# Kernel optimization log

Hardware: AMD Instinct MI355X
Metric: run time of the kernel (lower is better)

Reference implementation:

```python
import jax, jax.numpy as jnp
import numpy as np

B, C, N = 8, 128, 4096

def conv1x1(x, W, b):
    # x: [B, Cin, N], W: [Cout, Cin], b: [Cout] -> [B, Cout, N]
    return jnp.einsum('oc,bcn->bon', W, x) + b[None, :, None]

def setup_inputs() -> dict:
    key = jax.random.key(0)
    ks = jax.random.split(key, 9)
    s = 1.0 / np.sqrt(C)
    return {
        'x': jax.random.normal(ks[0], (B, C, N), dtype=jnp.float32),
        'Wq': jax.random.uniform(ks[1], (C, C), jnp.float32, -s, s),
        'bq': jax.random.uniform(ks[2], (C,), jnp.float32, -s, s),
        'Wk': jax.random.uniform(ks[3], (C, C), jnp.float32, -s, s),
        'bk': jax.random.uniform(ks[4], (C,), jnp.float32, -s, s),
        'Wv': jax.random.uniform(ks[5], (C, C), jnp.float32, -s, s),
        'bv': jax.random.uniform(ks[6], (C,), jnp.float32, -s, s),
        'Wf': jax.random.uniform(ks[7], (C, C), jnp.float32, -s, s),
        'bf': jax.random.uniform(ks[8], (C,), jnp.float32, -s, s),
    }

def reference(x, Wq, bq, Wk, bk, Wv, bv, Wf, bf):
    q = conv1x1(x, Wq, bq)  # [B, C, N]
    k = conv1x1(x, Wk, bk)
    v = conv1x1(x, Wv, bv)
    # scores[b, i, j] = sum_c q[b, c, i] * k[b, c, j]; softmax over j (no scaling, as in source)
    attn = jax.nn.softmax(jnp.einsum('bci,bcj->bij', q, k), axis=-1)  # [B, N, N]
    # out[b, c, i] = sum_j v[b, c, j] * attn[b, i, j]
    attn_out = jnp.einsum('bcj,bij->bci', v, attn)  # [B, C, N]
    return conv1x1(attn_out, Wf, bf) + x
```

## Files before the change

### kernel.cpp

```cpp
#include <hip/hip_runtime.h>
#include <cstdio>


#define BATCH 8
#define CH    128
#define NPOS  4096
#define BCN   (BATCH * CH * NPOS)
#define LOG2E 1.4426950408889634f

typedef __attribute__((ext_vector_type(8)))  short bf16x8;
typedef __attribute__((ext_vector_type(16))) float f32x16;
typedef unsigned short ushort_t;
typedef unsigned int   uint32;

#if __has_builtin(__builtin_amdgcn_exp2f)
#define EXP2(x) __builtin_amdgcn_exp2f(x)
#else
#define EXP2(x) exp2f(x)
#endif

__device__ inline ushort_t f2bf(float f) {
    uint32 u = __float_as_uint(f);
    u += 0x7FFFu + ((u >> 16) & 1u);
    return (ushort_t)(u >> 16);
}
__device__ inline float bf2f(ushort_t h) {
    return __uint_as_float(((uint32)h) << 16);
}
__device__ inline f32x16 z16() {
    f32x16 r;
#pragma unroll
    for (int i = 0; i < 16; ++i) r[i] = 0.f;
    return r;
}
__device__ inline void gl_lds16(const ushort_t* g, ushort_t* l) {
    __builtin_amdgcn_global_load_lds(
        (const __attribute__((address_space(1))) uint32*)g,
        (__attribute__((address_space(3))) uint32*)l, 16, 0, 0);
}
__device__ inline bf16x8 cvt8(const float* p, float s) {
    const float4 a = *(const float4*)p;
    const float4 c = *(const float4*)(p + 4);
    uint32 u0, u1, u2, u3;
    asm("v_cvt_pk_bf16_f32 %0, %1, %2" : "=v"(u0) : "v"(a.x * s), "v"(a.y * s));
    asm("v_cvt_pk_bf16_f32 %0, %1, %2" : "=v"(u1) : "v"(a.z * s), "v"(a.w * s));
    asm("v_cvt_pk_bf16_f32 %0, %1, %2" : "=v"(u2) : "v"(c.x * s), "v"(c.y * s));
    asm("v_cvt_pk_bf16_f32 %0, %1, %2" : "=v"(u3) : "v"(c.z * s), "v"(c.w * s));
    union { uint32 u[4]; bf16x8 v; } r;
    r.u[0] = u0; r.u[1] = u1; r.u[2] = u2; r.u[3] = u3;
    return r.v;
}
__device__ inline bf16x8 comb8(bf16x8 p0, bf16x8 p1, float s) {
    uint32 u[4];
#pragma unroll
    for (int i = 0; i < 4; ++i) {
        const float a = (bf2f((ushort_t)p0[2 * i])     + bf2f((ushort_t)p1[2 * i]))     * s;
        const float b = (bf2f((ushort_t)p0[2 * i + 1]) + bf2f((ushort_t)p1[2 * i + 1])) * s;
        asm("v_cvt_pk_bf16_f32 %0, %1, %2" : "=v"(u[i]) : "v"(a), "v"(b));
    }
    union { uint32 uu[4]; bf16x8 v; } r;
    r.uu[0] = u[0]; r.uu[1] = u[1]; r.uu[2] = u[2]; r.uu[3] = u[3];
    return r.v;
}

__global__ __launch_bounds__(256, 2)
void qkv_mfma_kernel(const float* __restrict__ x,
                     const float* __restrict__ Wq, const float* __restrict__ bq,
                     const float* __restrict__ Wk, const float* __restrict__ bk,
                     const float* __restrict__ Wv, const float* __restrict__ bv_,
                     ushort_t* __restrict__ qt, ushort_t* __restrict__ kt,
                     ushort_t* __restrict__ vb)
{
    __shared__ float    xs[32][69];
    __shared__ ushort_t xh[64][136];
    __shared__ ushort_t xl[64][136];

    const int blk = blockIdx.x;
    const int b   = blk & 7;
    const int n0  = (blk >> 3) * 64;

    const int tid = threadIdx.x;
    const int w   = tid >> 6;
    const int l   = tid & 63;
    const int l31 = l & 31;
    const int g2  = l >> 5;

    for (int c0 = 0; c0 < CH; c0 += 32) {
        __syncthreads();
        {
            const int r = tid >> 3, f4 = tid & 7;
            const size_t base = (size_t)(b * CH + c0 + r) * NPOS + n0;
            *(float4*)&xs[r][4 * f4]      = *(const float4*)&x[base + 4 * f4];
            *(float4*)&xs[r][32 + 4 * f4] = *(const float4*)&x[base + 32 + 4 * f4];
        }
        __syncthreads();
        {
            const int n = tid >> 2, oc = tid & 3;
            bf16x8 hi, lo;
#pragma unroll
            for (int m = 0; m < 8; ++m) {
                const float v = xs[oc * 8 + m][n];
                const ushort_t h = f2bf(v);
                hi[m] = (short)h;
                lo[m] = (short)f2bf(v - bf2f(h));
            }
            *(bf16x8*)&xh[n][c0 + oc * 8] = hi;
            *(bf16x8*)&xl[n][c0 + oc * 8] = lo;
        }
    }
    __syncthreads();

    f32x16 aq0 = z16(), aq1 = z16(), ak0 = z16(), ak1 = z16();
    f32x16 av0 = z16(), av1 = z16();
    const int co = w * 32 + l31;
    const size_t wrow = (size_t)co * CH;

#pragma unroll
    for (int k = 0; k < 8; ++k) {
        const int ko = k * 16 + g2 * 8;
        const bf16x8 xh0 = *(const bf16x8*)&xh[l31][ko];
        const bf16x8 xh1 = *(const bf16x8*)&xh[32 + l31][ko];
        const bf16x8 xl0 = *(const bf16x8*)&xl[l31][ko];
        const bf16x8 xl1 = *(const bf16x8*)&xl[32 + l31][ko];
        const bf16x8 wqf = cvt8(Wq + wrow + ko, 1.0f);
        const bf16x8 wkf = cvt8(Wk + wrow + ko, LOG2E);
        const bf16x8 wvf = cvt8(Wv + wrow + ko, 1.0f);

        aq0 = __builtin_amdgcn_mfma_f32_32x32x16_bf16(xh0, wqf, aq0, 0, 0, 0);
        aq0 = __builtin_amdgcn_mfma_f32_32x32x16_bf16(xl0, wqf, aq0, 0, 0, 0);
        aq1 = __builtin_amdgcn_mfma_f32_32x32x16_bf16(xh1, wqf, aq1, 0, 0, 0);
        aq1 = __builtin_amdgcn_mfma_f32_32x32x16_bf16(xl1, wqf, aq1, 0, 0, 0);
        ak0 = __builtin_amdgcn_mfma_f32_32x32x16_bf16(xh0, wkf, ak0, 0, 0, 0);
        ak0 = __builtin_amdgcn_mfma_f32_32x32x16_bf16(xl0, wkf, ak0, 0, 0, 0);
        ak1 = __builtin_amdgcn_mfma_f32_32x32x16_bf16(xh1, wkf, ak1, 0, 0, 0);
        ak1 = __builtin_amdgcn_mfma_f32_32x32x16_bf16(xl1, wkf, ak1, 0, 0, 0);
        av0 = __builtin_amdgcn_mfma_f32_32x32x16_bf16(wvf, xh0, av0, 0, 0, 0);
        av0 = __builtin_amdgcn_mfma_f32_32x32x16_bf16(wvf, xl0, av0, 0, 0, 0);
        av1 = __builtin_amdgcn_mfma_f32_32x32x16_bf16(wvf, xh1, av1, 0, 0, 0);
        av1 = __builtin_amdgcn_mfma_f32_32x32x16_bf16(wvf, xl1, av1, 0, 0, 0);
    }

    const float bqv = bq[co];
    const float bkv = bk[co] * LOG2E;
    ushort_t* qtb = qt + (size_t)b * NPOS * CH;
    ushort_t* ktb = kt + (size_t)b * NPOS * CH;
    ushort_t* vbb = vb + (size_t)b * CH * NPOS;

#pragma unroll
    for (int rg = 0; rg < 16; ++rg) {
        const int rr = (rg & 3) + 8 * (rg >> 2) + 4 * g2;
        {
            const int na = n0 + rr;
            const int nbr = n0 + 32 + rr;
            qtb[(size_t)na * CH + co]  = f2bf(aq0[rg] + bqv);
            qtb[(size_t)nbr * CH + co] = f2bf(aq1[rg] + bqv);
            ktb[(size_t)na * CH + co]  = f2bf(ak0[rg] + bkv);
            ktb[(size_t)nbr * CH + co] = f2bf(ak1[rg] + bkv);
        }
        {
            const int cov = w * 32 + rr;
            const float bvv = bv_[cov];
            vbb[(size_t)cov * NPOS + n0 + l31]      = f2bf(av0[rg] + bvv);
            vbb[(size_t)cov * NPOS + n0 + 32 + l31] = f2bf(av1[rg] + bvv);
        }
    }
}

__global__ __launch_bounds__(256, 2)
void attn_kernel(const ushort_t* __restrict__ qt, const ushort_t* __restrict__ kt,
                 const ushort_t* __restrict__ vb, ushort_t* __restrict__ pO,
                 float* __restrict__ lw)
{
    __shared__ ushort_t Sh[4 * 8192];

    const int blk = blockIdx.x;
    const int b   = blk & 7;
    const int r   = blk >> 3;
    const int it  = r & 31;
    const int sp  = r >> 5;

    const int tid = threadIdx.x;
    const int w   = tid >> 6;
    const int l   = tid & 63;
    const int l31 = l & 31;
    const int g2  = l >> 5;

    const size_t boff = (size_t)b * NPOS * CH;
    const ushort_t* qtb = qt + boff;
    const ushort_t* ktb = kt + boff;
    const ushort_t* vbb = vb + boff;

    const int i0  = it * 128;
    const int j0b = sp * (NPOS / 2);
    const int iw  = i0 + w * 32 + l31;

    auto stage = [&](int buf, int j0) {
        ushort_t* Kl = Sh + buf * 16384;
        ushort_t* Vl = Kl + 8192;
#pragma unroll
        for (int qq = 0; qq < 4; ++qq) {
            const int u = w * 256 + qq * 64 + l;
            {
                const int row = u >> 4, sl = u & 15;
                gl_lds16(ktb + (size_t)(j0 + row) * CH + ((sl ^ (row & 7)) << 3),
                         Kl + (w * 256 + qq * 64) * 8);
            }
            {
                const int c = u >> 3, sl = u & 7;
                gl_lds16(vbb + (size_t)c * NPOS + j0 + ((sl ^ (c & 7)) << 3),
                         Vl + (w * 256 + qq * 64) * 8);
            }
        }
    };

    stage(0, j0b);

    bf16x8 qa[8];
#pragma unroll
    for (int ck = 0; ck < 8; ++ck)
        qa[ck] = *(const bf16x8*)&qtb[(size_t)iw * CH + (ck * 2 + g2) * 8];

    __syncthreads();

    f32x16 o0 = z16(), o1 = z16(), o2 = z16(), o3 = z16();
    float lsum = 0.f;

    const int NT = (NPOS / 2) / 64;
    for (int t = 0; t < NT; ++t) {
        const int cur = t & 1;
        if (t + 1 < NT) stage(cur ^ 1, j0b + (t + 1) * 64);

        const ushort_t* Kl = Sh + cur * 16384;
        const ushort_t* Vl = Kl + 8192;

#pragma unroll
        for (int sub = 0; sub < 2; ++sub) {
            f32x16 sS = z16();
            const int krow  = sub * 32 + l31;
            const int kbase = krow * 128;
            const int ksw   = krow & 7;
            __builtin_amdgcn_s_setprio(1);
#pragma unroll
            for (int ck = 0; ck < 8; ++ck) {
                const bf16x8 ka =
                    *(const bf16x8*)&Kl[kbase + (((ck * 2 + g2) ^ ksw) << 3)];
                sS = __builtin_amdgcn_mfma_f32_32x32x16_bf16(ka, qa[ck], sS, 0, 0, 0);
            }
            __builtin_amdgcn_s_setprio(0);

            float p[16];
#pragma unroll
            for (int rg = 0; rg < 16; ++rg) {
                p[rg] = EXP2(sS[rg]);
                lsum += p[rg];
            }
            uint32 d[4][2];
#pragma unroll
            for (int qd = 0; qd < 4; ++qd)
#pragma unroll
                for (int td = 0; td < 2; ++td)
                    asm("v_cvt_pk_bf16_f32 %0, %1, %2"
                        : "=v"(d[qd][td])
                        : "v"(p[4 * qd + 2 * td]), "v"(p[4 * qd + 2 * td + 1]));

#pragma unroll
            for (int kcl = 0; kcl < 2; ++kcl) {
                uint32 a0 = d[2 * kcl][0], a1 = d[2 * kcl][1];
                uint32 b0 = d[2 * kcl + 1][0], b1 = d[2 * kcl + 1][1];
                asm("v_permlane32_swap_b32 %0, %1" : "+v"(a0), "+v"(b0));
                asm("v_permlane32_swap_b32 %0, %1" : "+v"(a1), "+v"(b1));
                union { uint32 u[4]; bf16x8 v; } pf;
                pf.u[0] = a0; pf.u[1] = a1; pf.u[2] = b0; pf.u[3] = b1;

                const int vsl = (sub * 2 + kcl) * 2 + g2;
                __builtin_amdgcn_s_setprio(1);
                {
                    const int c = l31;
                    const bf16x8 vv = *(const bf16x8*)&Vl[c * 64 + ((vsl ^ (c & 7)) << 3)];
                    o0 = __builtin_amdgcn_mfma_f32_32x32x16_bf16(pf.v, vv, o0, 0, 0, 0);
                }
                {
                    const int c = 32 + l31;
                    const bf16x8 vv = *(const bf16x8*)&Vl[c * 64 + ((vsl ^ (c & 7)) << 3)];
                    o1 = __builtin_amdgcn_mfma_f32_32x32x16_bf16(pf.v, vv, o1, 0, 0, 0);
                }
                {
                    const int c = 64 + l31;
                    const bf16x8 vv = *(const bf16x8*)&Vl[c * 64 + ((vsl ^ (c & 7)) << 3)];
                    o2 = __builtin_amdgcn_mfma_f32_32x32x16_bf16(pf.v, vv, o2, 0, 0, 0);
                }
                {
                    const int c = 96 + l31;
                    const bf16x8 vv = *(const bf16x8*)&Vl[c * 64 + ((vsl ^ (c & 7)) << 3)];
                    o3 = __builtin_amdgcn_mfma_f32_32x32x16_bf16(pf.v, vv, o3, 0, 0, 0);
                }
                __builtin_amdgcn_s_setprio(0);
            }
        }
        __syncthreads();
    }

    const float lpart = lsum + __shfl_xor(lsum, 32);
    ushort_t* pOb = pO + (size_t)sp * BCN + boff;
    float* lwb = lw + (size_t)sp * (BATCH * NPOS) + (size_t)b * NPOS;
#pragma unroll
    for (int rg = 0; rg < 16; ++rg) {
        const int rr = (rg & 3) + 8 * (rg >> 2) + 4 * g2;
        const int n  = i0 + w * 32 + rr;
        ushort_t* rowp = pOb + (size_t)n * CH;
        rowp[l31]      = f2bf(o0[rg]);
        rowp[32 + l31] = f2bf(o1[rg]);
        rowp[64 + l31] = f2bf(o2[rg]);
        rowp[96 + l31] = f2bf(o3[rg]);
    }
    if (l < 32) lwb[i0 + w * 32 + l] = lpart;
}

__global__ __launch_bounds__(256, 2)
void final_mfma_kernel(const ushort_t* __restrict__ pO, const float* __restrict__ lw,
                       const float* __restrict__ Wf, const float* __restrict__ bf_,
                       const float* __restrict__ x, float* __restrict__ out)
{
    const int blk = blockIdx.x;
    const int b   = blk & 7;
    const int n0  = (blk >> 3) * 64;

    const int tid = threadIdx.x;
    const int w   = tid >> 6;
    const int l   = tid & 63;
    const int l31 = l & 31;
    const int g2  = l >> 5;

    const int BN = BATCH * NPOS;
    const int co = w * 32 + l31;
    const size_t wrow = (size_t)co * CH;

    const int bn0 = b * NPOS + n0 + l31;
    const int bn1 = bn0 + 32;
    const float invl0 = 1.0f / (lw[bn0] + lw[BN + bn0]);
    const float invl1 = 1.0f / (lw[bn1] + lw[BN + bn1]);

    f32x16 a0 = z16(), a1 = z16();

#pragma unroll
    for (int k = 0; k < 8; ++k) {
        const int ko = k * 16 + g2 * 8;
        const bf16x8 wf = cvt8(Wf + wrow + ko, 1.0f);
        {
            const size_t base = (size_t)bn0 * CH + ko;
            const bf16x8 p0 = *(const bf16x8*)&pO[base];
            const bf16x8 p1 = *(const bf16x8*)&pO[base + (size_t)BCN];
            const bf16x8 aof = comb8(p0, p1, invl0);
            a0 = __builtin_amdgcn_mfma_f32_32x32x16_bf16(wf, aof, a0, 0, 0, 0);
        }
        {
            const size_t base = (size_t)bn1 * CH + ko;
            const bf16x8 p0 = *(const bf16x8*)&pO[base];
            const bf16x8 p1 = *(const bf16x8*)&pO[base + (size_t)BCN];
            const bf16x8 aof = comb8(p0, p1, invl1);
            a1 = __builtin_amdgcn_mfma_f32_32x32x16_bf16(wf, aof, a1, 0, 0, 0);
        }
    }

#pragma unroll
    for (int rg = 0; rg < 16; ++rg) {
        const int rr  = (rg & 3) + 8 * (rg >> 2) + 4 * g2;
        const int cov = w * 32 + rr;
        const float bfv = bf_[cov];
        const size_t rbase = (size_t)(b * CH + cov) * NPOS + n0;
        out[rbase + l31]      = a0[rg] + bfv + x[rbase + l31];
        out[rbase + 32 + l31] = a1[rg] + bfv + x[rbase + 32 + l31];
    }
}

extern "C" void kernel_launch(void* const* d_in, const int* in_sizes, int n_in,
                              void* d_out, int out_size, void* d_ws, size_t ws_size,
                              hipStream_t stream)
{
    (void)in_sizes; (void)n_in; (void)out_size;
    const float* x  = (const float*)d_in[0];
    const float* Wq = (const float*)d_in[1];
    const float* bq = (const float*)d_in[2];
    const float* Wk = (const float*)d_in[3];
    const float* bk = (const float*)d_in[4];
    const float* Wv = (const float*)d_in[5];
    const float* bv = (const float*)d_in[6];
    const float* Wf = (const float*)d_in[7];
    const float* bf = (const float*)d_in[8];
    float* out = (float*)d_out;

    const size_t MB = 1u << 20;
    const size_t need = 40 * MB + 256 * 1024;
    if (ws_size < need) {
        fprintf(stderr, "kernel_launch: ws_size %zu < needed %zu\n", ws_size, need);
        return;
    }
    char* wsc = (char*)d_ws;
    ushort_t* qt   = (ushort_t*)(wsc + 0);
    ushort_t* kt   = (ushort_t*)(wsc + 8 * MB);
    ushort_t* vbuf = (ushort_t*)(wsc + 16 * MB);
    ushort_t* pO   = (ushort_t*)(wsc + 24 * MB);
    float*    lw   = (float*)(wsc + 40 * MB);

    qkv_mfma_kernel<<<dim3(512), 256, 0, stream>>>(
        x, Wq, bq, Wk, bk, Wv, bv, qt, kt, vbuf);
    attn_kernel<<<dim3(512), 256, 0, stream>>>(qt, kt, vbuf, pO, lw);
    final_mfma_kernel<<<dim3(512), 256, 0, stream>>>(
        pO, lw, Wf, bf, x, out);
}
```

Baseline: 111.2 us.

## Double query rows per warp, split keys four ways, stream swizzled Q from global

Each warp in the attention kernel now handles 64 query rows instead of 32. Every K and V fragment loaded into LDS is therefore reused across two MFMA chains, which halves LDS traffic per FLOP. To keep 512 blocks, the key dimension is split into four partitions instead of two, and the final kernel sums four partial outputs and denominators. Q is written in a fragment-swizzled layout and read from global (cache) inside the inner loop rather than held in registers. This costs more partial-output memory traffic, more accumulator registers (risking spills at 2 waves), and repeated Q loads.

```diff
diff --git a/kernel.cpp b/kernel.cpp
--- a/kernel.cpp
+++ b/kernel.cpp
@@ -50,12 +50,14 @@
     r.u[0] = u0; r.u[1] = u1; r.u[2] = u2; r.u[3] = u3;
     return r.v;
 }
-__device__ inline bf16x8 comb8(bf16x8 p0, bf16x8 p1, float s) {
+__device__ inline bf16x8 comb4(bf16x8 p0, bf16x8 p1, bf16x8 p2, bf16x8 p3, float s) {
     uint32 u[4];
 #pragma unroll
     for (int i = 0; i < 4; ++i) {
-        const float a = (bf2f((ushort_t)p0[2 * i])     + bf2f((ushort_t)p1[2 * i]))     * s;
-        const float b = (bf2f((ushort_t)p0[2 * i + 1]) + bf2f((ushort_t)p1[2 * i + 1])) * s;
+        const float a = (bf2f((ushort_t)p0[2 * i]) + bf2f((ushort_t)p1[2 * i]) +
+                         bf2f((ushort_t)p2[2 * i]) + bf2f((ushort_t)p3[2 * i])) * s;
+        const float b = (bf2f((ushort_t)p0[2 * i + 1]) + bf2f((ushort_t)p1[2 * i + 1]) +
+                         bf2f((ushort_t)p2[2 * i + 1]) + bf2f((ushort_t)p3[2 * i + 1])) * s;
         asm("v_cvt_pk_bf16_f32 %0, %1, %2" : "=v"(u[i]) : "v"(a), "v"(b));
     }
     union { uint32 uu[4]; bf16x8 v; } r;
@@ -150,12 +152,16 @@
     for (int rg = 0; rg < 16; ++rg) {
         const int rr = (rg & 3) + 8 * (rg >> 2) + 4 * g2;
         {
-            const int na = n0 + rr;
-            const int nbr = n0 + 32 + rr;
-            qtb[(size_t)na * CH + co]  = f2bf(aq0[rg] + bqv);
-            qtb[(size_t)nbr * CH + co] = f2bf(aq1[rg] + bqv);
+            const int na  = n0 + rr;
+            const int nb2 = n0 + 32 + rr;
+            const uint32 offa = (uint32)(((na >> 5) * 16 + (co >> 3)) << 8) +
+                                ((na & 31) << 3) + (co & 7);
+            const uint32 offb = (uint32)(((nb2 >> 5) * 16 + (co >> 3)) << 8) +
+                                ((nb2 & 31) << 3) + (co & 7);
+            qtb[offa] = f2bf(aq0[rg] + bqv);
+            qtb[offb] = f2bf(aq1[rg] + bqv);
             ktb[(size_t)na * CH + co]  = f2bf(ak0[rg] + bkv);
-            ktb[(size_t)nbr * CH + co] = f2bf(ak1[rg] + bkv);
+            ktb[(size_t)nb2 * CH + co] = f2bf(ak1[rg] + bkv);
         }
         {
             const int cov = w * 32 + rr;
@@ -167,7 +173,7 @@
 }
 
 __global__ __launch_bounds__(256, 2)
-void attn_kernel(const ushort_t* __restrict__ qt, const ushort_t* __restrict__ kt,
+void attn_kernel(const ushort_t* __restrict__ qsw, const ushort_t* __restrict__ kt,
                  const ushort_t* __restrict__ vb, ushort_t* __restrict__ pO,
                  float* __restrict__ lw)
 {
@@ -176,8 +182,8 @@
     const int blk = blockIdx.x;
     const int b   = blk & 7;
     const int r   = blk >> 3;
-    const int it  = r & 31;
-    const int sp  = r >> 5;
+    const int it  = r & 15;
+    const int sp  = r >> 4;
 
     const int tid = threadIdx.x;
     const int w   = tid >> 6;
@@ -186,13 +192,16 @@
     const int g2  = l >> 5;
 
     const size_t boff = (size_t)b * NPOS * CH;
-    const ushort_t* qtb = qt + boff;
     const ushort_t* ktb = kt + boff;
     const ushort_t* vbb = vb + boff;
 
-    const int i0  = it * 128;
-    const int j0b = sp * (NPOS / 2);
-    const int iw  = i0 + w * 32 + l31;
+    const int i0  = it * 256;
+    const int iw0 = i0 + w * 64;
+    const int j0b = sp * (NPOS / 4);
+
+    const ushort_t* qlane = qsw + boff + (size_t)l * 8;
+    const uint32 qb0 = (uint32)(((i0 >> 5) + 2 * w) * 16) << 8;
+    const uint32 qb1 = qb0 + (16u << 8);
 
     auto stage = [&](int buf, int j0) {
         ushort_t* Kl = Sh + buf * 16384;
@@ -214,18 +223,16 @@
     };
 
     stage(0, j0b);
-
-    bf16x8 qa[8];
-#pragma unroll
-    for (int ck = 0; ck < 8; ++ck)
-        qa[ck] = *(const bf16x8*)&qtb[(size_t)iw * CH + (ck * 2 + g2) * 8];
-
     __syncthreads();
 
-    f32x16 o0 = z16(), o1 = z16(), o2 = z16(), o3 = z16();
-    float lsum = 0.f;
-
-    const int NT = (NPOS / 2) / 64;
+    f32x16 o[2][4];
+#pragma unroll
+    for (int ib = 0; ib < 2; ++ib)
+#pragma unroll
+        for (int cb = 0; cb < 4; ++cb) o[ib][cb] = z16();
+    float lsum[2] = {0.f, 0.f};
+
+    const int NT = (NPOS / 4) / 64;
     for (int t = 0; t < NT; ++t) {
         const int cur = t & 1;
         if (t + 1 < NT) stage(cur ^ 1, j0b + (t + 1) * 64);
@@ -235,64 +242,60 @@
 
 #pragma unroll
         for (int sub = 0; sub < 2; ++sub) {
-            f32x16 sS = z16();
+            f32x16 s0 = z16(), s1 = z16();
             const int krow  = sub * 32 + l31;
             const int kbase = krow * 128;
             const int ksw   = krow & 7;
-            __builtin_amdgcn_s_setprio(1);
-#pragma unroll
+#pragma unroll 2
             for (int ck = 0; ck < 8; ++ck) {
+                const bf16x8 q0 = *(const bf16x8*)&qlane[qb0 + ck * 512];
+                const bf16x8 q1 = *(const bf16x8*)&qlane[qb1 + ck * 512];
                 const bf16x8 ka =
                     *(const bf16x8*)&Kl[kbase + (((ck * 2 + g2) ^ ksw) << 3)];
-                sS = __builtin_amdgcn_mfma_f32_32x32x16_bf16(ka, qa[ck], sS, 0, 0, 0);
-            }
-            __builtin_amdgcn_s_setprio(0);
-
-            float p[16];
-#pragma unroll
-            for (int rg = 0; rg < 16; ++rg) {
-                p[rg] = EXP2(sS[rg]);
-                lsum += p[rg];
-            }
-            uint32 d[4][2];
-#pragma unroll
-            for (int qd = 0; qd < 4; ++qd)
-#pragma unroll
-                for (int td = 0; td < 2; ++td)
-                    asm("v_cvt_pk_bf16_f32 %0, %1, %2"
-                        : "=v"(d[qd][td])
-                        : "v"(p[4 * qd + 2 * td]), "v"(p[4 * qd + 2 * td + 1]));
+                s0 = __builtin_amdgcn_mfma_f32_32x32x16_bf16(ka, q0, s0, 0, 0, 0);
+                s1 = __builtin_amdgcn_mfma_f32_32x32x16_bf16(ka, q1, s1, 0, 0, 0);
+            }
+
+            uint32 d[2][4][2];
+#pragma unroll
+            for (int ib = 0; ib < 2; ++ib) {
+                float p[16];
+#pragma unroll
+                for (int rg = 0; rg < 16; ++rg) {
+                    p[rg] = EXP2(ib == 0 ? s0[rg] : s1[rg]);
+                    lsum[ib] += p[rg];
+                }
+#pragma unroll
+                for (int qd = 0; qd < 4; ++qd)
+#pragma unroll
+                    for (int td = 0; td < 2; ++td)
+                        asm("v_cvt_pk_bf16_f32 %0, %1, %2"
+                            : "=v"(d[ib][qd][td])
+                            : "v"(p[4 * qd + 2 * td]), "v"(p[4 * qd + 2 * td + 1]));
+            }
 
 #pragma unroll
             for (int kcl = 0; kcl < 2; ++kcl) {
-                uint32 a0 = d[2 * kcl][0], a1 = d[2 * kcl][1];
-                uint32 b0 = d[2 * kcl + 1][0], b1 = d[2 * kcl + 1][1];
-                asm("v_permlane32_swap_b32 %0, %1" : "+v"(a0), "+v"(b0));
-                asm("v_permlane32_swap_b32 %0, %1" : "+v"(a1), "+v"(b1));
-                union { uint32 u[4]; bf16x8 v; } pf;
-                pf.u[0] = a0; pf.u[1] = a1; pf.u[2] = b0; pf.u[3] = b1;
-
+                bf16x8 pf[2];
+#pragma unroll
+                for (int ib = 0; ib < 2; ++ib) {
+                    uint32 a0 = d[ib][2 * kcl][0],     a1 = d[ib][2 * kcl][1];
+                    uint32 b0 = d[ib][2 * kcl + 1][0], b1 = d[ib][2 * kcl + 1][1];
+                    asm("v_permlane32_swap_b32 %0, %1" : "+v"(a0), "+v"(b0));
+                    asm("v_permlane32_swap_b32 %0, %1" : "+v"(a1), "+v"(b1));
+                    union { uint32 u[4]; bf16x8 v; } pu;
+                    pu.u[0] = a0; pu.u[1] = a1; pu.u[2] = b0; pu.u[3] = b1;
+                    pf[ib] = pu.v;
+                }
                 const int vsl = (sub * 2 + kcl) * 2 + g2;
                 __builtin_amdgcn_s_setprio(1);
-                {
-                    const int c = l31;
-                    const bf16x8 vv = *(const bf16x8*)&Vl[c * 64 + ((vsl ^ (c & 7)) << 3)];
-                    o0 = __builtin_amdgcn_mfma_f32_32x32x16_bf16(pf.v, vv, o0, 0, 0, 0);
-                }
-                {
-                    const int c = 32 + l31;
-                    const bf16x8 vv = *(const bf16x8*)&Vl[c * 64 + ((vsl ^ (c & 7)) << 3)];
-                    o1 = __builtin_amdgcn_mfma_f32_32x32x16_bf16(pf.v, vv, o1, 0, 0, 0);
-                }
-                {
-                    const int c = 64 + l31;
-                    const bf16x8 vv = *(const bf16x8*)&Vl[c * 64 + ((vsl ^ (c & 7)) << 3)];
-                    o2 = __builtin_amdgcn_mfma_f32_32x32x16_bf16(pf.v, vv, o2, 0, 0, 0);
-                }
-                {
-                    const int c = 96 + l31;
-                    const bf16x8 vv = *(const bf16x8*)&Vl[c * 64 + ((vsl ^ (c & 7)) << 3)];
-                    o3 = __builtin_amdgcn_mfma_f32_32x32x16_bf16(pf.v, vv, o3, 0, 0, 0);
+#pragma unroll
+                for (int cb = 0; cb < 4; ++cb) {
+                    const int c = cb * 32 + l31;
+                    const bf16x8 vv =
+                        *(const bf16x8*)&Vl[c * 64 + ((vsl ^ (c & 7)) << 3)];
+                    o[0][cb] = __builtin_amdgcn_mfma_f32_32x32x16_bf16(pf[0], vv, o[0][cb], 0, 0, 0);
+                    o[1][cb] = __builtin_amdgcn_mfma_f32_32x32x16_bf16(pf[1], vv, o[1][cb], 0, 0, 0);
                 }
                 __builtin_amdgcn_s_setprio(0);
             }
@@ -300,20 +303,27 @@
         __syncthreads();
     }
 
-    const float lpart = lsum + __shfl_xor(lsum, 32);
+    float lp0 = lsum[0] + __shfl_xor(lsum[0], 32);
+    float lp1 = lsum[1] + __shfl_xor(lsum[1], 32);
     ushort_t* pOb = pO + (size_t)sp * BCN + boff;
     float* lwb = lw + (size_t)sp * (BATCH * NPOS) + (size_t)b * NPOS;
 #pragma unroll
     for (int rg = 0; rg < 16; ++rg) {
         const int rr = (rg & 3) + 8 * (rg >> 2) + 4 * g2;
-        const int n  = i0 + w * 32 + rr;
-        ushort_t* rowp = pOb + (size_t)n * CH;
-        rowp[l31]      = f2bf(o0[rg]);
-        rowp[32 + l31] = f2bf(o1[rg]);
-        rowp[64 + l31] = f2bf(o2[rg]);
-        rowp[96 + l31] = f2bf(o3[rg]);
-    }
-    if (l < 32) lwb[i0 + w * 32 + l] = lpart;
+#pragma unroll
+        for (int ib = 0; ib < 2; ++ib) {
+            const int n = iw0 + ib * 32 + rr;
+            ushort_t* rowp = pOb + (size_t)n * CH;
+            rowp[l31]      = f2bf(o[ib][0][rg]);
+            rowp[32 + l31] = f2bf(o[ib][1][rg]);
+            rowp[64 + l31] = f2bf(o[ib][2][rg]);
+            rowp[96 + l31] = f2bf(o[ib][3][rg]);
+        }
+    }
+    if (l < 32) {
+        lwb[iw0 + l]      = lp0;
+        lwb[iw0 + 32 + l] = lp1;
+    }
 }
 
 __global__ __launch_bounds__(256, 2)
@@ -337,8 +347,8 @@
 
     const int bn0 = b * NPOS + n0 + l31;
     const int bn1 = bn0 + 32;
-    const float invl0 = 1.0f / (lw[bn0] + lw[BN + bn0]);
-    const float invl1 = 1.0f / (lw[bn1] + lw[BN + bn1]);
+    const float invl0 = 1.0f / (lw[bn0] + lw[BN + bn0] + lw[2 * BN + bn0] + lw[3 * BN + bn0]);
+    const float invl1 = 1.0f / (lw[bn1] + lw[BN + bn1] + lw[2 * BN + bn1] + lw[3 * BN + bn1]);
 
     f32x16 a0 = z16(), a1 = z16();
 
@@ -350,14 +360,18 @@
             const size_t base = (size_t)bn0 * CH + ko;
             const bf16x8 p0 = *(const bf16x8*)&pO[base];
             const bf16x8 p1 = *(const bf16x8*)&pO[base + (size_t)BCN];
-            const bf16x8 aof = comb8(p0, p1, invl0);
+            const bf16x8 p2 = *(const bf16x8*)&pO[base + (size_t)2 * BCN];
+            const bf16x8 p3 = *(const bf16x8*)&pO[base + (size_t)3 * BCN];
+            const bf16x8 aof = comb4(p0, p1, p2, p3, invl0);
             a0 = __builtin_amdgcn_mfma_f32_32x32x16_bf16(wf, aof, a0, 0, 0, 0);
         }
         {
             const size_t base = (size_t)bn1 * CH + ko;
             const bf16x8 p0 = *(const bf16x8*)&pO[base];
             const bf16x8 p1 = *(const bf16x8*)&pO[base + (size_t)BCN];
-            const bf16x8 aof = comb8(p0, p1, invl1);
+            const bf16x8 p2 = *(const bf16x8*)&pO[base + (size_t)2 * BCN];
+            const bf16x8 p3 = *(const bf16x8*)&pO[base + (size_t)3 * BCN];
+            const bf16x8 aof = comb4(p0, p1, p2, p3, invl1);
             a1 = __builtin_amdgcn_mfma_f32_32x32x16_bf16(wf, aof, a1, 0, 0, 0);
         }
     }
@@ -390,7 +404,7 @@
     float* out = (float*)d_out;
 
     const size_t MB = 1u << 20;
-    const size_t need = 40 * MB + 256 * 1024;
+    const size_t need = 56 * MB + 512 * 1024;
     if (ws_size < need) {
         fprintf(stderr, "kernel_launch: ws_size %zu < needed %zu\n", ws_size, need);
         return;
@@ -400,7 +414,7 @@
     ushort_t* kt   = (ushort_t*)(wsc + 8 * MB);
     ushort_t* vbuf = (ushort_t*)(wsc + 16 * MB);
     ushort_t* pO   = (ushort_t*)(wsc + 24 * MB);
-    float*    lw   = (float*)(wsc + 40 * MB);
+    float*    lw   = (float*)(wsc + 56 * MB);
 
     qkv_mfma_kernel<<<dim3(512), 256, 0, stream>>>(
         x, Wq, bq, Wk, bk, Wv, bv, qt, kt, vbuf);
```

Measured after the change: 132.7 us. 1.19x slower.

## Split attention key range four ways with smaller KV tiles and higher occupancy

Applied to the files above, without the earlier changes.

The attention kernel now splits the key/value range into four partitions instead of two, doubling the grid to 1024 blocks. It also halves the per-iteration KV tile to 32 keys, shrinking LDS and raising the occupancy hint to 4 blocks per CU. The final kernel combines four partial outputs and four partial row sums. This trades more parallelism and latency hiding for twice the partial-output traffic to global memory and more sync iterations per key.

```diff
diff --git a/kernel.cpp b/kernel.cpp
--- a/kernel.cpp
+++ b/kernel.cpp
@@ -50,12 +50,14 @@
     r.u[0] = u0; r.u[1] = u1; r.u[2] = u2; r.u[3] = u3;
     return r.v;
 }
-__device__ inline bf16x8 comb8(bf16x8 p0, bf16x8 p1, float s) {
+__device__ inline bf16x8 comb4(bf16x8 p0, bf16x8 p1, bf16x8 p2, bf16x8 p3, float s) {
     uint32 u[4];
 #pragma unroll
     for (int i = 0; i < 4; ++i) {
-        const float a = (bf2f((ushort_t)p0[2 * i])     + bf2f((ushort_t)p1[2 * i]))     * s;
-        const float b = (bf2f((ushort_t)p0[2 * i + 1]) + bf2f((ushort_t)p1[2 * i + 1])) * s;
+        const float a = (bf2f((ushort_t)p0[2 * i]) + bf2f((ushort_t)p1[2 * i]) +
+                         bf2f((ushort_t)p2[2 * i]) + bf2f((ushort_t)p3[2 * i])) * s;
+        const float b = (bf2f((ushort_t)p0[2 * i + 1]) + bf2f((ushort_t)p1[2 * i + 1]) +
+                         bf2f((ushort_t)p2[2 * i + 1]) + bf2f((ushort_t)p3[2 * i + 1])) * s;
         asm("v_cvt_pk_bf16_f32 %0, %1, %2" : "=v"(u[i]) : "v"(a), "v"(b));
     }
     union { uint32 uu[4]; bf16x8 v; } r;
@@ -166,12 +168,12 @@
     }
 }
 
-__global__ __launch_bounds__(256, 2)
+__global__ __launch_bounds__(256, 4)
 void attn_kernel(const ushort_t* __restrict__ qt, const ushort_t* __restrict__ kt,
                  const ushort_t* __restrict__ vb, ushort_t* __restrict__ pO,
                  float* __restrict__ lw)
 {
-    __shared__ ushort_t Sh[4 * 8192];
+    __shared__ ushort_t Sh[2 * 8192];
 
     const int blk = blockIdx.x;
     const int b   = blk & 7;
@@ -191,24 +193,24 @@
     const ushort_t* vbb = vb + boff;
 
     const int i0  = it * 128;
-    const int j0b = sp * (NPOS / 2);
+    const int j0b = sp * (NPOS / 4);
     const int iw  = i0 + w * 32 + l31;
 
     auto stage = [&](int buf, int j0) {
-        ushort_t* Kl = Sh + buf * 16384;
-        ushort_t* Vl = Kl + 8192;
-#pragma unroll
-        for (int qq = 0; qq < 4; ++qq) {
-            const int u = w * 256 + qq * 64 + l;
+        ushort_t* Kl = Sh + buf * 8192;
+        ushort_t* Vl = Kl + 4096;
+#pragma unroll
+        for (int qq = 0; qq < 2; ++qq) {
+            const int u = qq * 256 + w * 64 + l;
             {
                 const int row = u >> 4, sl = u & 15;
                 gl_lds16(ktb + (size_t)(j0 + row) * CH + ((sl ^ (row & 7)) << 3),
-                         Kl + (w * 256 + qq * 64) * 8);
-            }
-            {
-                const int c = u >> 3, sl = u & 7;
-                gl_lds16(vbb + (size_t)c * NPOS + j0 + ((sl ^ (c & 7)) << 3),
-                         Vl + (w * 256 + qq * 64) * 8);
+                         Kl + (qq * 256 + w * 64) * 8);
+            }
+            {
+                const int c = u >> 2, sl = u & 3;
+                gl_lds16(vbb + (size_t)c * NPOS + j0 + ((sl ^ ((c >> 1) & 3)) << 3),
+                         Vl + (qq * 256 + w * 64) * 8);
             }
         }
     };
@@ -225,77 +227,73 @@
     f32x16 o0 = z16(), o1 = z16(), o2 = z16(), o3 = z16();
     float lsum = 0.f;
 
-    const int NT = (NPOS / 2) / 64;
+    const int NT = (NPOS / 4) / 32;
     for (int t = 0; t < NT; ++t) {
         const int cur = t & 1;
-        if (t + 1 < NT) stage(cur ^ 1, j0b + (t + 1) * 64);
-
-        const ushort_t* Kl = Sh + cur * 16384;
-        const ushort_t* Vl = Kl + 8192;
-
-#pragma unroll
-        for (int sub = 0; sub < 2; ++sub) {
-            f32x16 sS = z16();
-            const int krow  = sub * 32 + l31;
-            const int kbase = krow * 128;
-            const int ksw   = krow & 7;
+        if (t + 1 < NT) stage(cur ^ 1, j0b + (t + 1) * 32);
+
+        const ushort_t* Kl = Sh + cur * 8192;
+        const ushort_t* Vl = Kl + 4096;
+
+        f32x16 sS = z16();
+        const int kbase = l31 * 128;
+        const int ksw   = l31 & 7;
+        __builtin_amdgcn_s_setprio(1);
+#pragma unroll
+        for (int ck = 0; ck < 8; ++ck) {
+            const bf16x8 ka =
+                *(const bf16x8*)&Kl[kbase + (((ck * 2 + g2) ^ ksw) << 3)];
+            sS = __builtin_amdgcn_mfma_f32_32x32x16_bf16(ka, qa[ck], sS, 0, 0, 0);
+        }
+        __builtin_amdgcn_s_setprio(0);
+
+        float p[16];
+#pragma unroll
+        for (int rg = 0; rg < 16; ++rg) {
+            p[rg] = EXP2(sS[rg]);
+            lsum += p[rg];
+        }
+        uint32 d[4][2];
+#pragma unroll
+        for (int qd = 0; qd < 4; ++qd)
+#pragma unroll
+            for (int td = 0; td < 2; ++td)
+                asm("v_cvt_pk_bf16_f32 %0, %1, %2"
+                    : "=v"(d[qd][td])
+                    : "v"(p[4 * qd + 2 * td]), "v"(p[4 * qd + 2 * td + 1]));
+
+#pragma unroll
+        for (int kcl = 0; kcl < 2; ++kcl) {
+            uint32 a0 = d[2 * kcl][0], a1 = d[2 * kcl][1];
+            uint32 b0 = d[2 * kcl + 1][0], b1 = d[2 * kcl + 1][1];
+            asm("v_permlane32_swap_b32 %0, %1" : "+v"(a0), "+v"(b0));
+            asm("v_permlane32_swap_b32 %0, %1" : "+v"(a1), "+v"(b1));
+            union { uint32 u[4]; bf16x8 v; } pf;
+            pf.u[0] = a0; pf.u[1] = a1; pf.u[2] = b0; pf.u[3] = b1;
+
+            const int vsl = kcl * 2 + g2;
             __builtin_amdgcn_s_setprio(1);
-#pragma unroll
-            for (int ck = 0; ck < 8; ++ck) {
-                const bf16x8 ka =
-                    *(const bf16x8*)&Kl[kbase + (((ck * 2 + g2) ^ ksw) << 3)];
-                sS = __builtin_amdgcn_mfma_f32_32x32x16_bf16(ka, qa[ck], sS, 0, 0, 0);
+            {
+                const int c = l31;
+                const bf16x8 vv = *(const bf16x8*)&Vl[c * 32 + ((vsl ^ ((c >> 1) & 3)) << 3)];
+                o0 = __builtin_amdgcn_mfma_f32_32x32x16_bf16(pf.v, vv, o0, 0, 0, 0);
+            }
+            {
+                const int c = 32 + l31;
+                const bf16x8 vv = *(const bf16x8*)&Vl[c * 32 + ((vsl ^ ((c >> 1) & 3)) << 3)];
+                o1 = __builtin_amdgcn_mfma_f32_32x32x16_bf16(pf.v, vv, o1, 0, 0, 0);
+            }
+            {
+                const int c = 64 + l31;
+                const bf16x8 vv = *(const bf16x8*)&Vl[c * 32 + ((vsl ^ ((c >> 1) & 3)) << 3)];
+                o2 = __builtin_amdgcn_mfma_f32_32x32x16_bf16(pf.v, vv, o2, 0, 0, 0);
+            }
+            {
+                const int c = 96 + l31;
+                const bf16x8 vv = *(const bf16x8*)&Vl[c * 32 + ((vsl ^ ((c >> 1) & 3)) << 3)];
+                o3 = __builtin_amdgcn_mfma_f32_32x32x16_bf16(pf.v, vv, o3, 0, 0, 0);
             }
             __builtin_amdgcn_s_setprio(0);
-
-            float p[16];
-#pragma unroll
-            for (int rg = 0; rg < 16; ++rg) {
-                p[rg] = EXP2(sS[rg]);
-                lsum += p[rg];
-            }
-            uint32 d[4][2];
-#pragma unroll
-            for (int qd = 0; qd < 4; ++qd)
-#pragma unroll
-                for (int td = 0; td < 2; ++td)
-                    asm("v_cvt_pk_bf16_f32 %0, %1, %2"
-                        : "=v"(d[qd][td])
-                        : "v"(p[4 * qd + 2 * td]), "v"(p[4 * qd + 2 * td + 1]));
-
-#pragma unroll
-            for (int kcl = 0; kcl < 2; ++kcl) {
-                uint32 a0 = d[2 * kcl][0], a1 = d[2 * kcl][1];
-                uint32 b0 = d[2 * kcl + 1][0], b1 = d[2 * kcl + 1][1];
-                asm("v_permlane32_swap_b32 %0, %1" : "+v"(a0), "+v"(b0));
-                asm("v_permlane32_swap_b32 %0, %1" : "+v"(a1), "+v"(b1));
-                union { uint32 u[4]; bf16x8 v; } pf;
-                pf.u[0] = a0; pf.u[1] = a1; pf.u[2] = b0; pf.u[3] = b1;
-
-                const int vsl = (sub * 2 + kcl) * 2 + g2;
-                __builtin_amdgcn_s_setprio(1);
-                {
-                    const int c = l31;
-                    const bf16x8 vv = *(const bf16x8*)&Vl[c * 64 + ((vsl ^ (c & 7)) << 3)];
-                    o0 = __builtin_amdgcn_mfma_f32_32x32x16_bf16(pf.v, vv, o0, 0, 0, 0);
-                }
-                {
-                    const int c = 32 + l31;
-                    const bf16x8 vv = *(const bf16x8*)&Vl[c * 64 + ((vsl ^ (c & 7)) << 3)];
-                    o1 = __builtin_amdgcn_mfma_f32_32x32x16_bf16(pf.v, vv, o1, 0, 0, 0);
-                }
-                {
-                    const int c = 64 + l31;
-                    const bf16x8 vv = *(const bf16x8*)&Vl[c * 64 + ((vsl ^ (c & 7)) << 3)];
-                    o2 = __builtin_amdgcn_mfma_f32_32x32x16_bf16(pf.v, vv, o2, 0, 0, 0);
-                }
-                {
-                    const int c = 96 + l31;
-                    const bf16x8 vv = *(const bf16x8*)&Vl[c * 64 + ((vsl ^ (c & 7)) << 3)];
-                    o3 = __builtin_amdgcn_mfma_f32_32x32x16_bf16(pf.v, vv, o3, 0, 0, 0);
-                }
-                __builtin_amdgcn_s_setprio(0);
-            }
         }
         __syncthreads();
     }
@@ -337,8 +335,8 @@
 
     const int bn0 = b * NPOS + n0 + l31;
     const int bn1 = bn0 + 32;
-    const float invl0 = 1.0f / (lw[bn0] + lw[BN + bn0]);
-    const float invl1 = 1.0f / (lw[bn1] + lw[BN + bn1]);
+    const float invl0 = 1.0f / (lw[bn0] + lw[BN + bn0] + lw[2 * BN + bn0] + lw[3 * BN + bn0]);
+    const float invl1 = 1.0f / (lw[bn1] + lw[BN + bn1] + lw[2 * BN + bn1] + lw[3 * BN + bn1]);
 
     f32x16 a0 = z16(), a1 = z16();
 
@@ -350,14 +348,18 @@
             const size_t base = (size_t)bn0 * CH + ko;
             const bf16x8 p0 = *(const bf16x8*)&pO[base];
             const bf16x8 p1 = *(const bf16x8*)&pO[base + (size_t)BCN];
-            const bf16x8 aof = comb8(p0, p1, invl0);
+            const bf16x8 p2 = *(const bf16x8*)&pO[base + (size_t)2 * BCN];
+            const bf16x8 p3 = *(const bf16x8*)&pO[base + (size_t)3 * BCN];
+            const bf16x8 aof = comb4(p0, p1, p2, p3, invl0);
             a0 = __builtin_amdgcn_mfma_f32_32x32x16_bf16(wf, aof, a0, 0, 0, 0);
         }
         {
             const size_t base = (size_t)bn1 * CH + ko;
             const bf16x8 p0 = *(const bf16x8*)&pO[base];
             const bf16x8 p1 = *(const bf16x8*)&pO[base + (size_t)BCN];
-            const bf16x8 aof = comb8(p0, p1, invl1);
+            const bf16x8 p2 = *(const bf16x8*)&pO[base + (size_t)2 * BCN];
+            const bf16x8 p3 = *(const bf16x8*)&pO[base + (size_t)3 * BCN];
+            const bf16x8 aof = comb4(p0, p1, p2, p3, invl1);
             a1 = __builtin_amdgcn_mfma_f32_32x32x16_bf16(wf, aof, a1, 0, 0, 0);
         }
     }
@@ -390,7 +392,7 @@
     float* out = (float*)d_out;
 
     const size_t MB = 1u << 20;
-    const size_t need = 40 * MB + 256 * 1024;
+    const size_t need = 56 * MB + 512 * 1024;
     if (ws_size < need) {
         fprintf(stderr, "kernel_launch: ws_size %zu < needed %zu\n", ws_size, need);
         return;
@@ -400,11 +402,11 @@
     ushort_t* kt   = (ushort_t*)(wsc + 8 * MB);
     ushort_t* vbuf = (ushort_t*)(wsc + 16 * MB);
     ushort_t* pO   = (ushort_t*)(wsc + 24 * MB);
-    float*    lw   = (float*)(wsc + 40 * MB);
+    float*    lw   = (float*)(wsc + 56 * MB);
 
     qkv_mfma_kernel<<<dim3(512), 256, 0, stream>>>(
         x, Wq, bq, Wk, bk, Wv, bv, qt, kt, vbuf);
-    attn_kernel<<<dim3(512), 256, 0, stream>>>(qt, kt, vbuf, pO, lw);
+    attn_kernel<<<dim3(1024), 256, 0, stream>>>(qt, kt, vbuf, pO, lw);
     final_mfma_kernel<<<dim3(512), 256, 0, stream>>>(
         pO, lw, Wf, bf, x, out);
 }
```

After: 154.9 us. 1.39x slower.
